# Performance work log

Measured on AMD Instinct MI355X. Metric: run time of the kernel, lower is better.

The kernel has to match this reference:

```python
import jax, jax.numpy as jnp
import numpy as np

B, V = 256, 128000

def setup_inputs() -> dict:
    key = jax.random.key(0)
    k0, k1, k2, k3, k4, k5 = jax.random.split(key, 6)
    logits = jax.random.normal(k0, (B, V), dtype=jnp.float32) * 2.0
    temperatures = jax.random.uniform(k1, (B,), dtype=jnp.float32, minval=0.5, maxval=1.5)
    top_ks = jax.random.randint(k2, (B,), 1, 64, dtype=jnp.int32)
    top_ps = jax.random.uniform(k3, (B,), dtype=jnp.float32, minval=0.8, maxval=1.0)
    min_ps = jax.random.uniform(k4, (B,), dtype=jnp.float32, minval=0.0, maxval=0.1)
    uniform_noise = jax.random.uniform(k5, (B,), dtype=jnp.float32)
    return dict(logits=logits, temperatures=temperatures, top_ks=top_ks,
                top_ps=top_ps, min_ps=min_ps, uniform_noise=uniform_noise)

def _renorm(p):
    return p / jnp.sum(p, axis=-1, keepdims=True)

def _top_k_renorm(probs, top_ks):
    # keep the k largest probs per row, renormalize
    sorted_desc = jnp.sort(probs, axis=-1)[:, ::-1]           # [B,V]
    k_idx = jnp.clip(jnp.maximum(top_ks, 1) - 1, 0, probs.shape[-1] - 1)
    kth = jnp.take_along_axis(sorted_desc, k_idx[:, None], axis=-1)  # [B,1]
    return _renorm(jnp.where(probs >= kth, probs, 0.0))

def _top_p_renorm(probs, top_ps):
    # keep the smallest prefix of sorted probs whose mass covers top_p
    sorted_desc = jnp.sort(probs, axis=-1)[:, ::-1]
    csum = jnp.cumsum(sorted_desc, axis=-1)
    keep = (csum - sorted_desc) < top_ps[:, None]             # cumulative mass before token < p
    thresh = jnp.min(jnp.where(keep, sorted_desc, jnp.inf), axis=-1, keepdims=True)
    return _renorm(jnp.where(probs >= thresh, probs, 0.0))

def _min_p_sample(probs, min_ps, u):
    # keep tokens with prob >= min_p * max_prob, renormalize, inverse-CDF sample
    max_p = jnp.max(probs, axis=-1, keepdims=True)
    probs = _renorm(jnp.where(probs >= min_ps[:, None] * max_p, probs, 0.0))
    cdf = jnp.cumsum(probs, axis=-1)
    target = u[:, None] * cdf[:, -1:]
    tokens = jnp.argmax(cdf >= target, axis=-1).astype(jnp.int32)
    return tokens, probs

def reference(logits, temperatures, top_ks, top_ps, min_ps, uniform_noise):
    probs = jax.nn.softmax(logits.astype(jnp.float32) / temperatures[:, None], axis=-1)
    probs = _top_k_renorm(probs, top_ks)
    probs = _top_p_renorm(probs, top_ps)
    tokens, probs = _min_p_sample(probs, min_ps, uniform_noise)
    return tokens, probs
```

## Files before the change

kernel.cpp:

```cpp
#include <hip/hip_runtime.h>
#include <cmath>


constexpr int BB   = 256;
constexpr int VV   = 128000;
constexpr int CAP  = 512;
constexpr int NVEC = VV / 4;
constexpr int IPL  = CAP / 64;

__global__ __launch_bounds__(1024) void k_fused(
    const float* __restrict__ logits, const float* __restrict__ temps,
    const int* __restrict__ topks, const float* __restrict__ topps,
    const float* __restrict__ minps, const float* __restrict__ noise,
    float* __restrict__ out) {
  const int row = blockIdx.x;
  const int tid = threadIdx.x;
  const float* lrow = logits + (size_t)row * VV;
  float* orow = out + BB + (size_t)row * VV;

  __shared__ float cl[CAP];
  __shared__ int   ci[CAP];
  __shared__ int   s_cnt;
  __shared__ float s_t, s_lo, s_hi, s_max;
  __shared__ float wmax[16];

  if (tid == 0) s_cnt = 0;
  __syncthreads();

  const float4* lp4 = reinterpret_cast<const float4*>(lrow);
  float4* op4 = reinterpret_cast<float4*>(orow);
  const float4 z4 = make_float4(0.f, 0.f, 0.f, 0.f);
  const float T0 = 6.0f;

  float m = -INFINITY;
  for (int j = tid; j < NVEC; j += 1024) {
    const float4 v = lp4[j];
    op4[j] = z4;
    m = fmaxf(fmaxf(fmaxf(v.x, v.y), fmaxf(v.z, v.w)), m);
    const int base = j << 2;
    if (v.x >= T0) { int p = atomicAdd(&s_cnt, 1); if (p < CAP) { cl[p] = v.x; ci[p] = base;     } }
    if (v.y >= T0) { int p = atomicAdd(&s_cnt, 1); if (p < CAP) { cl[p] = v.y; ci[p] = base + 1; } }
    if (v.z >= T0) { int p = atomicAdd(&s_cnt, 1); if (p < CAP) { cl[p] = v.z; ci[p] = base + 2; } }
    if (v.w >= T0) { int p = atomicAdd(&s_cnt, 1); if (p < CAP) { cl[p] = v.w; ci[p] = base + 3; } }
  }
  for (int o = 32; o > 0; o >>= 1) m = fmaxf(m, __shfl_xor(m, o, 64));
  if ((tid & 63) == 0) wmax[tid >> 6] = m;
  __syncthreads();
  if (tid == 0) {
    float mm = wmax[0];
    for (int i = 1; i < 16; ++i) mm = fmaxf(mm, wmax[i]);
    s_max = mm;
    s_lo = mm - 40.0f;
    s_hi = mm + 1.0f;
  }
  __syncthreads();
  int cnt = s_cnt;

  float tcur = T0;
  for (int it = 0; it < 24 && (cnt < 64 || cnt > CAP); ++it) {
    if (tid == 0) {
      if (cnt > CAP) s_lo = tcur; else s_hi = tcur;
      s_t = 0.5f * (s_lo + s_hi);
      s_cnt = 0;
    }
    __syncthreads();
    tcur = s_t;
    for (int j = tid; j < NVEC; j += 1024) {
      const float4 v = lp4[j];
      const int base = j << 2;
      if (v.x >= tcur) { int p = atomicAdd(&s_cnt, 1); if (p < CAP) { cl[p] = v.x; ci[p] = base;     } }
      if (v.y >= tcur) { int p = atomicAdd(&s_cnt, 1); if (p < CAP) { cl[p] = v.y; ci[p] = base + 1; } }
      if (v.z >= tcur) { int p = atomicAdd(&s_cnt, 1); if (p < CAP) { cl[p] = v.z; ci[p] = base + 2; } }
      if (v.w >= tcur) { int p = atomicAdd(&s_cnt, 1); if (p < CAP) { cl[p] = v.w; ci[p] = base + 3; } }
    }
    __syncthreads();
    cnt = s_cnt;
  }
  const int n = min(cnt, CAP);

  if (tid < 64) {
    const int lane = tid;
    float rv[IPL]; int rix[IPL];
#pragma unroll
    for (int q = 0; q < IPL; ++q) {
      const int idx = lane + (q << 6);
      const bool ok = idx < n;
      rv[q]  = ok ? cl[idx] : -INFINITY;
      rix[q] = ok ? ci[idx] : 0x7fffffff;
    }
    const int n64 = min(n, 64);
    float lv = 0.0f; int iv = 0x7fffffff;
    for (int r = 0; r < n64; ++r) {
      float bv = rv[0]; int bi = rix[0];
#pragma unroll
      for (int q = 1; q < IPL; ++q) if (rv[q] > bv) { bv = rv[q]; bi = rix[q]; }
      for (int o = 32; o > 0; o >>= 1) {
        const float ov = __shfl_xor(bv, o, 64);
        const int   oi = __shfl_xor(bi, o, 64);
        if (ov > bv || (ov == bv && oi < bi)) { bv = ov; bi = oi; }
      }
#pragma unroll
      for (int q = 0; q < IPL; ++q) if (rix[q] == bi) { rv[q] = -INFINITY; rix[q] = 0x7fffffff; }
      if (lane == r) { lv = bv; iv = bi; }
    }

    const float Tv = temps[row];
    const float Mx = s_max / Tv;
    const bool valid = lane < n64;
    const float p = valid ? expf(lv / Tv - Mx) : 0.0f;

    int k = topks[row];
    k = max(1, min(k, n64));
    const float kth = __shfl(p, k - 1, 64);
    const bool keepA = valid && (p >= kth);
    float S1 = keepA ? p : 0.0f;
    for (int o = 32; o > 0; o >>= 1) S1 += __shfl_xor(S1, o, 64);
    const float q = keepA ? (p / S1) : 0.0f;

    float cs = q;
    for (int o = 1; o < 64; o <<= 1) { const float v = __shfl_up(cs, o, 64); if (lane >= o) cs += v; }
    const float lhs = cs - q;
    const bool keepBp = keepA && (lhs < topps[row]);
    float thr = keepBp ? q : INFINITY;
    for (int o = 32; o > 0; o >>= 1) thr = fminf(thr, __shfl_xor(thr, o, 64));
    const bool keepB = keepA && (q >= thr);
    float S2 = keepB ? q : 0.0f;
    for (int o = 32; o > 0; o >>= 1) S2 += __shfl_xor(S2, o, 64);
    const float r2 = keepB ? (q / S2) : 0.0f;

    const float r0 = __shfl(r2, 0, 64);
    const bool keepC = keepB && (r2 >= minps[row] * r0);
    float S3 = keepC ? r2 : 0.0f;
    for (int o = 32; o > 0; o >>= 1) S3 += __shfl_xor(S3, o, 64);
    const float f = keepC ? (r2 / S3) : 0.0f;

    float cum = 0.0f, tot = 0.0f;
    for (int i2 = 0; i2 < 64; ++i2) {
      const float fi = __shfl(f, i2, 64);
      const int   ii = __shfl(iv, i2, 64);
      tot += fi;
      if (ii <= iv) cum += fi;
    }
    const float target = noise[row] * tot;
    int tok = 0;
    if (target > 0.0f) {
      int cand = (keepC && cum >= target) ? iv : 0x7fffffff;
      for (int o = 32; o > 0; o >>= 1) cand = min(cand, __shfl_xor(cand, o, 64));
      if (cand == 0x7fffffff) {
        int mi = keepC ? iv : -1;
        for (int o = 32; o > 0; o >>= 1) mi = max(mi, __shfl_xor(mi, o, 64));
        cand = (mi < 0) ? 0 : mi;
      }
      tok = cand;
    }

    if (keepC) orow[iv] = f;
    if (lane == 0) out[row] = (float)tok;
  }
}

extern "C" void kernel_launch(void* const* d_in, const int* in_sizes, int n_in,
                              void* d_out, int out_size, void* d_ws, size_t ws_size,
                              hipStream_t stream) {
  const float* logits = (const float*)d_in[0];
  const float* temps  = (const float*)d_in[1];
  const int*   topks  = (const int*)d_in[2];
  const float* topps  = (const float*)d_in[3];
  const float* minps  = (const float*)d_in[4];
  const float* noise  = (const float*)d_in[5];
  float* out = (float*)d_out;

  k_fused<<<BB, 1024, 0, stream>>>(logits, temps, topks, topps, minps, noise, out);
}
```

Before: 282.3 us.

## Split fused per-row kernel into grid-wide streaming pass plus per-row select

The single 256-block kernel, one block per row, is replaced by three launches. A zeroing kernel clears per-row counters. A 4000-block streaming kernel reads the logits, writes zeros to the output and appends candidates at or above a fixed threshold into per-row workspace buffers through global atomics. A per-row select kernel then loads those candidates and falls back to rescanning its row only when the count is out of range. The aim is to use the whole GPU for the bandwidth-bound pass instead of 256 blocks, and to take the row max from the top candidate rather than a full reduction. The cost is two extra launches and global atomic contention, and the fallback bisection now uses an open-ended bracket.

```diff
diff --git a/kernel.cpp b/kernel.cpp
--- a/kernel.cpp
+++ b/kernel.cpp
@@ -2,79 +2,92 @@
 #include <cmath>
 
 
-constexpr int BB   = 256;
-constexpr int VV   = 128000;
-constexpr int CAP  = 512;
-constexpr int NVEC = VV / 4;
-constexpr int IPL  = CAP / 64;
+constexpr int BB  = 256;
+constexpr int VV  = 128000;
+constexpr int CAP = 512;
+constexpr int IPL = CAP / 64;
+constexpr int NV4_ROW = VV / 4;
+constexpr int K1_THREADS = 256;
+constexpr int K1_BLOCKS  = 4000;
+constexpr int K1_STRIDE  = K1_THREADS * K1_BLOCKS;
+constexpr int K1_ROWSTRIDE = K1_STRIDE / NV4_ROW;
+constexpr int K1_UNR = 8;
+constexpr float T0 = 6.0f;
 
-__global__ __launch_bounds__(1024) void k_fused(
+__global__ void k_zero(int* __restrict__ gcnt) { gcnt[threadIdx.x] = 0; }
+
+__global__ __launch_bounds__(K1_THREADS) void k_stream(
+    const float* __restrict__ logits, float* __restrict__ out,
+    int* __restrict__ gcnt, float* __restrict__ gcl, int* __restrict__ gix) {
+  const int idx  = blockIdx.x * K1_THREADS + threadIdx.x;
+  const int row0 = idx / NV4_ROW;
+  const int col  = (idx - row0 * NV4_ROW) << 2;
+  const float4* in4 = reinterpret_cast<const float4*>(logits);
+  float4* o4 = reinterpret_cast<float4*>(out + BB);
+
+  float4 v[K1_UNR];
+#pragma unroll
+  for (int u = 0; u < K1_UNR; ++u) v[u] = in4[idx + u * K1_STRIDE];
+  const float4 z = make_float4(0.f, 0.f, 0.f, 0.f);
+#pragma unroll
+  for (int u = 0; u < K1_UNR; ++u) o4[idx + u * K1_STRIDE] = z;
+#pragma unroll
+  for (int u = 0; u < K1_UNR; ++u) {
+    const float4 vv = v[u];
+    if (vv.x >= T0 || vv.y >= T0 || vv.z >= T0 || vv.w >= T0) {
+      const int row = row0 + u * K1_ROWSTRIDE;
+      if (vv.x >= T0) { int p = atomicAdd(&gcnt[row], 1); if (p < CAP) { gcl[row*CAP+p] = vv.x; gix[row*CAP+p] = col;     } }
+      if (vv.y >= T0) { int p = atomicAdd(&gcnt[row], 1); if (p < CAP) { gcl[row*CAP+p] = vv.y; gix[row*CAP+p] = col + 1; } }
+      if (vv.z >= T0) { int p = atomicAdd(&gcnt[row], 1); if (p < CAP) { gcl[row*CAP+p] = vv.z; gix[row*CAP+p] = col + 2; } }
+      if (vv.w >= T0) { int p = atomicAdd(&gcnt[row], 1); if (p < CAP) { gcl[row*CAP+p] = vv.w; gix[row*CAP+p] = col + 3; } }
+    }
+  }
+}
+
+__global__ __launch_bounds__(256) void k_select(
     const float* __restrict__ logits, const float* __restrict__ temps,
     const int* __restrict__ topks, const float* __restrict__ topps,
     const float* __restrict__ minps, const float* __restrict__ noise,
-    float* __restrict__ out) {
+    const int* __restrict__ gcnt, const float* __restrict__ gcl,
+    const int* __restrict__ gix, float* __restrict__ out) {
   const int row = blockIdx.x;
   const int tid = threadIdx.x;
-  const float* lrow = logits + (size_t)row * VV;
   float* orow = out + BB + (size_t)row * VV;
 
   __shared__ float cl[CAP];
   __shared__ int   ci[CAP];
   __shared__ int   s_cnt;
-  __shared__ float s_t, s_lo, s_hi, s_max;
-  __shared__ float wmax[16];
+  __shared__ float s_t, s_lo, s_hi;
 
-  if (tid == 0) s_cnt = 0;
+  int cnt = gcnt[row];
+  const int n0 = min(cnt, CAP);
+  for (int i = tid; i < n0; i += 256) { cl[i] = gcl[row*CAP+i]; ci[i] = gix[row*CAP+i]; }
   __syncthreads();
 
-  const float4* lp4 = reinterpret_cast<const float4*>(lrow);
-  float4* op4 = reinterpret_cast<float4*>(orow);
-  const float4 z4 = make_float4(0.f, 0.f, 0.f, 0.f);
-  const float T0 = 6.0f;
-
-  float m = -INFINITY;
-  for (int j = tid; j < NVEC; j += 1024) {
-    const float4 v = lp4[j];
-    op4[j] = z4;
-    m = fmaxf(fmaxf(fmaxf(v.x, v.y), fmaxf(v.z, v.w)), m);
-    const int base = j << 2;
-    if (v.x >= T0) { int p = atomicAdd(&s_cnt, 1); if (p < CAP) { cl[p] = v.x; ci[p] = base;     } }
-    if (v.y >= T0) { int p = atomicAdd(&s_cnt, 1); if (p < CAP) { cl[p] = v.y; ci[p] = base + 1; } }
-    if (v.z >= T0) { int p = atomicAdd(&s_cnt, 1); if (p < CAP) { cl[p] = v.z; ci[p] = base + 2; } }
-    if (v.w >= T0) { int p = atomicAdd(&s_cnt, 1); if (p < CAP) { cl[p] = v.w; ci[p] = base + 3; } }
-  }
-  for (int o = 32; o > 0; o >>= 1) m = fmaxf(m, __shfl_xor(m, o, 64));
-  if ((tid & 63) == 0) wmax[tid >> 6] = m;
-  __syncthreads();
-  if (tid == 0) {
-    float mm = wmax[0];
-    for (int i = 1; i < 16; ++i) mm = fmaxf(mm, wmax[i]);
-    s_max = mm;
-    s_lo = mm - 40.0f;
-    s_hi = mm + 1.0f;
-  }
-  __syncthreads();
-  int cnt = s_cnt;
-
-  float tcur = T0;
-  for (int it = 0; it < 24 && (cnt < 64 || cnt > CAP); ++it) {
-    if (tid == 0) {
-      if (cnt > CAP) s_lo = tcur; else s_hi = tcur;
-      s_t = 0.5f * (s_lo + s_hi);
-      s_cnt = 0;
+  if (cnt < 64 || cnt > CAP) {
+    const float4* lp4 = reinterpret_cast<const float4*>(logits + (size_t)row * VV);
+    if (tid == 0) { s_lo = (cnt > CAP) ? T0 : -1e30f; s_hi = (cnt > CAP) ? 1e30f : T0; }
+    __syncthreads();
+    for (int it = 0; it < 48 && (cnt < 64 || cnt > CAP); ++it) {
+      if (tid == 0) {
+        const float lo = s_lo, hi = s_hi;
+        s_t = (lo <= -1e29f) ? hi - 8.0f : (hi >= 1e29f ? lo + 8.0f : 0.5f * (lo + hi));
+        s_cnt = 0;
+      }
+      __syncthreads();
+      const float t = s_t;
+      for (int j = tid; j < NV4_ROW; j += 256) {
+        const float4 v = lp4[j]; const int base = j << 2;
+        if (v.x >= t) { int p = atomicAdd(&s_cnt, 1); if (p < CAP) { cl[p] = v.x; ci[p] = base;     } }
+        if (v.y >= t) { int p = atomicAdd(&s_cnt, 1); if (p < CAP) { cl[p] = v.y; ci[p] = base + 1; } }
+        if (v.z >= t) { int p = atomicAdd(&s_cnt, 1); if (p < CAP) { cl[p] = v.z; ci[p] = base + 2; } }
+        if (v.w >= t) { int p = atomicAdd(&s_cnt, 1); if (p < CAP) { cl[p] = v.w; ci[p] = base + 3; } }
+      }
+      __syncthreads();
+      cnt = s_cnt;
+      if (tid == 0) { if (cnt > CAP) s_lo = s_t; else if (cnt < 64) s_hi = s_t; }
+      __syncthreads();
     }
-    __syncthreads();
-    tcur = s_t;
-    for (int j = tid; j < NVEC; j += 1024) {
-      const float4 v = lp4[j];
-      const int base = j << 2;
-      if (v.x >= tcur) { int p = atomicAdd(&s_cnt, 1); if (p < CAP) { cl[p] = v.x; ci[p] = base;     } }
-      if (v.y >= tcur) { int p = atomicAdd(&s_cnt, 1); if (p < CAP) { cl[p] = v.y; ci[p] = base + 1; } }
-      if (v.z >= tcur) { int p = atomicAdd(&s_cnt, 1); if (p < CAP) { cl[p] = v.z; ci[p] = base + 2; } }
-      if (v.w >= tcur) { int p = atomicAdd(&s_cnt, 1); if (p < CAP) { cl[p] = v.w; ci[p] = base + 3; } }
-    }
-    __syncthreads();
-    cnt = s_cnt;
   }
   const int n = min(cnt, CAP);
 
@@ -105,7 +118,7 @@
     }
 
     const float Tv = temps[row];
-    const float Mx = s_max / Tv;
+    const float Mx = __shfl(lv, 0, 64) / Tv;
     const bool valid = lane < n64;
     const float p = valid ? expf(lv / Tv - Mx) : 0.0f;
 
@@ -170,5 +183,12 @@
   const float* noise  = (const float*)d_in[5];
   float* out = (float*)d_out;
 
-  k_fused<<<BB, 1024, 0, stream>>>(logits, temps, topks, topps, minps, noise, out);
+  int*   gcnt = (int*)d_ws;
+  float* gcl  = (float*)((char*)d_ws + 256 * sizeof(int));
+  int*   gix  = (int*)((char*)d_ws + 256 * sizeof(int) + (size_t)BB * CAP * sizeof(float));
+
+  k_zero<<<1, 256, 0, stream>>>(gcnt);
+  k_stream<<<K1_BLOCKS, K1_THREADS, 0, stream>>>(logits, out, gcnt, gcl, gix);
+  k_select<<<BB, 256, 0, stream>>>(logits, temps, topks, topps, minps, noise,
+                                   gcnt, gcl, gix, out);
 }
```

New measurement: 297.6 us. 5.4% more time.
